# Optimization experiments

Hardware: AMD Instinct MI355X
Metric: run time of the kernel (lower is better)

Reference implementation:

```python
import jax, jax.numpy as jnp
import numpy as np

N = 84          # nodes; N*(N-1)/2 == 3486, hardcoded by LayerNorm shapes
P = 3486        # number of pairwise rows
H = 2048        # h_size
EPS = 1e-5


def _gru_cell(x, h, Wih, Whh, bih, bhh):
    # PyTorch GRUCell math. Wih: [3H, in], Whh: [3H, H]
    gi = x @ Wih.T + bih
    gh = h @ Whh.T + bhh
    ir, iz, inew = jnp.split(gi, 3, axis=1)
    hr, hz, hnew = jnp.split(gh, 3, axis=1)
    r = jax.nn.sigmoid(ir + hr)
    z = jax.nn.sigmoid(iz + hz)
    n = jnp.tanh(inew + r * hnew)
    return (1.0 - z) * n + z * h


def _full_ln(x, w, b):
    # nn.LayerNorm([3486, h]) normalizes over BOTH dims jointly (biased var)
    mu = jnp.mean(x)
    var = jnp.mean((x - mu) ** 2)
    return (x - mu) * jax.lax.rsqrt(var + EPS) * w + b


def setup_inputs() -> dict:
    key = jax.random.key(0)
    ks = jax.random.split(key, 22)
    f32 = jnp.float32

    def nrm(k, shape, std):
        return jax.random.normal(k, shape, dtype=f32) * std

    h2 = H // 2
    return {
        "x": nrm(ks[0], (N, 64), 1.0),
        "hid": nrm(ks[1], (P, H), 1.0),
        # GRUCell(64, H) parameters
        "gru_Wih": nrm(ks[2], (3 * H, 64), 1.0 / np.sqrt(64)),
        "gru_Whh": nrm(ks[3], (3 * H, H), 1.0 / np.sqrt(H)),
        "gru_bih": nrm(ks[4], (3 * H,), 0.01),
        "gru_bhh": nrm(ks[5], (3 * H,), 0.01),
        # Linear/LayerNorm stack
        "W1": nrm(ks[6], (H, H), np.sqrt(2.0 / H)),
        "b1": jnp.zeros((H,), f32),
        "ln1_w": jnp.ones((P, H), f32),
        "ln1_b": jnp.zeros((P, H), f32),
        "W2": nrm(ks[7], (h2, H), np.sqrt(2.0 / H)),
        "b2": jnp.zeros((h2,), f32),
        "ln2_w": jnp.ones((P, h2), f32),
        "ln2_b": jnp.zeros((P, h2), f32),
        "W3": nrm(ks[8], (h2, h2), np.sqrt(2.0 / h2)),
        "b3": jnp.zeros((h2,), f32),
        "ln3_w": jnp.ones((P, h2), f32),
        "ln3_b": jnp.zeros((P, h2), f32),
        "W4": nrm(ks[9], (1, h2), np.sqrt(2.0 / h2)),
        "b4": jnp.zeros((1,), f32),
    }


def reference(x, hid, gru_Wih, gru_Whh, gru_bih, gru_bhh,
              W1, b1, ln1_w, ln1_b, W2, b2, ln2_w, ln2_b,
              W3, b3, ln3_w, ln3_b, W4, b4):
    # Pairwise gather: rows ordered (0,1),(0,2),...,(0,N-1),(1,2),... -- matches
    # the torch loop of expand+cat.
    iu, ju = jnp.triu_indices(N, k=1)
    x1 = x[iu]  # [P, 64]
    x2 = x[ju]  # [P, 64]

    h = _gru_cell(x1, hid, gru_Wih, gru_Whh, gru_bih, gru_bhh)
    h = _gru_cell(x2, h, gru_Wih, gru_Whh, gru_bih, gru_bhh)

    h = _full_ln(jax.nn.relu(h @ W1.T + b1), ln1_w, ln1_b)
    h = _full_ln(jax.nn.relu(h @ W2.T + b2), ln2_w, ln2_b)
    h = _full_ln(jax.nn.relu(h @ W3.T + b3), ln3_w, ln3_b)
    vals = jax.nn.sigmoid(h @ W4.T + b4)[:, 0]  # [P]

    # Strict-upper-triangular scatter + symmetrize (equals the torch pad loop)
    M = jnp.zeros((N, N), dtype=vals.dtype).at[iu, ju].set(vals)
    return M + M.T
```

## Files before the change

kernel.cpp:

```cpp
#include <hip/hip_runtime.h>
#include <stdint.h>

#define P_PAIRS 3486
#define NNODES 84
#define HSZ 2048
#define H2SZ 1024
#define G3H 6144
#define LN_EPS 1e-5f

typedef short bf16x8 __attribute__((ext_vector_type(8)));
typedef float f32x4 __attribute__((ext_vector_type(4)));

typedef __attribute__((address_space(3))) unsigned int lds_uint;
typedef __attribute__((address_space(1))) const unsigned int global_cuint;

__device__ __forceinline__ unsigned short f2bf(float f) {
    unsigned int u = __float_as_uint(f);
    return (unsigned short)((u + 0x7fffu + ((u >> 16) & 1u)) >> 16);
}
__device__ __forceinline__ float bf2f(unsigned short s) {
    return __uint_as_float(((unsigned int)s) << 16);
}
__device__ __forceinline__ float sigm(float x) {
    return 1.f / (1.f + expf(-x));
}

#define S_WHH (G3H * HSZ / 4)
#define S_W1  (HSZ * HSZ / 4)
#define S_W2  (H2SZ * HSZ / 4)
#define S_W3  (H2SZ * H2SZ / 4)
#define S_HID (P_PAIRS * HSZ / 4)
#define B0 (S_WHH)
#define B1 (B0 + S_W1)
#define B2 (B1 + S_W2)
#define B3 (B2 + S_W3)
#define B4 (B3 + S_HID)

__device__ __forceinline__ void cvt4(const float4* in, ushort4* out, int i) {
    float4 v = in[i];
    ushort4 o;
    o.x = f2bf(v.x); o.y = f2bf(v.y); o.z = f2bf(v.z); o.w = f2bf(v.w);
    out[i] = o;
}

__global__ void k_prep(const float4* __restrict__ Whh, ushort4* __restrict__ whh_b,
                       const float4* __restrict__ W1, ushort4* __restrict__ w1_b,
                       const float4* __restrict__ W2, ushort4* __restrict__ w2_b,
                       const float4* __restrict__ W3, ushort4* __restrict__ w3_b,
                       const float4* __restrict__ hid, ushort4* __restrict__ hid_b,
                       int* __restrict__ ip, int* __restrict__ jp, float* __restrict__ acc) {
    int idx = blockIdx.x * blockDim.x + threadIdx.x;
    if (idx < 8) acc[idx] = 0.f;
    if (idx < P_PAIRS) {
        int i = 0, rem = idx;
        while (rem >= NNODES - 1 - i) { rem -= NNODES - 1 - i; ++i; }
        ip[idx] = i;
        jp[idx] = i + 1 + rem;
    }
    int stride = gridDim.x * blockDim.x;
    for (; idx < B4; idx += stride) {
        if (idx < B0)      cvt4(Whh, whh_b, idx);
        else if (idx < B1) cvt4(W1, w1_b, idx - B0);
        else if (idx < B2) cvt4(W2, w2_b, idx - B1);
        else if (idx < B3) cvt4(W3, w3_b, idx - B2);
        else               cvt4(hid, hid_b, idx - B3);
    }
}

__global__ void k_gi(const float* __restrict__ x, const float* __restrict__ Wih,
                     const float* __restrict__ bih, float* __restrict__ gi) {
    int idx = blockIdx.x * blockDim.x + threadIdx.x;
    if (idx >= NNODES * G3H) return;
    int node = idx / G3H, n = idx - node * G3H;
    const float* xr = x + node * 64;
    const float* wr = Wih + (size_t)n * 64;
    float s = bih[n];
#pragma unroll
    for (int k = 0; k < 64; ++k) s += xr[k] * wr[k];
    gi[idx] = s;
}

__global__ __launch_bounds__(256)
void k_gemm(const unsigned short* __restrict__ A, const unsigned short* __restrict__ B,
            const float* __restrict__ bias, float* __restrict__ Cf,
            unsigned short* __restrict__ Cb,
            int M, int N, int K, int relu, float* __restrict__ accg, int redslot) {
    __shared__ __align__(16) unsigned short lsA[128 * 32];
    __shared__ __align__(16) unsigned short lsB[128 * 32];
    const int mt_count = (M + 127) >> 7;
    const int per_group = mt_count << 3;
    const int g = blockIdx.x / per_group;
    const int rr = blockIdx.x - g * per_group;
    const int nt = (g << 3) + (rr & 7);
    const int mt = rr >> 3;
    const int m0 = mt * 128;
    const int n0 = nt * 128;
    const int tid = threadIdx.x;
    const int lane = tid & 63;
    const int wave = tid >> 6;
    const int wr = (wave >> 1) * 64;
    const int wc = (wave & 1) * 64;
    const int fr = lane & 15;
    const int quad = lane >> 4;
    const int kof = quad * 8;

    f32x4 acc[4][4];
#pragma unroll
    for (int i = 0; i < 4; ++i)
#pragma unroll
        for (int j = 0; j < 4; ++j) {
            f32x4 z = {0.f, 0.f, 0.f, 0.f};
            acc[i][j] = z;
        }

    const int lin0 = (wave * 2) * 1024 + lane * 16;
    const int lin1 = lin0 + 1024;
    const int row0 = lin0 >> 6, col0 = (lin0 & 63) >> 1;
    const int row1 = lin1 >> 6, col1 = (lin1 & 63) >> 1;
    int ga0 = m0 + row0; if (ga0 >= M) ga0 = M - 1;
    int ga1 = m0 + row1; if (ga1 >= M) ga1 = M - 1;
    const int gb0 = n0 + row0, gb1 = n0 + row1;

    const unsigned short* pa0 = A + (size_t)ga0 * K + col0;
    const unsigned short* pa1 = A + (size_t)ga1 * K + col1;
    const unsigned short* pb0 = B + (size_t)gb0 * K + col0;
    const unsigned short* pb1 = B + (size_t)gb1 * K + col1;
    lds_uint* la0 = (lds_uint*)&lsA[(wave * 2) * 512];
    lds_uint* la1 = (lds_uint*)&lsA[(wave * 2 + 1) * 512];
    lds_uint* lb0 = (lds_uint*)&lsB[(wave * 2) * 512];
    lds_uint* lb1 = (lds_uint*)&lsB[(wave * 2 + 1) * 512];

    for (int k0 = 0; k0 < K; k0 += 32) {
        __syncthreads();
        __builtin_amdgcn_global_load_lds((global_cuint*)(pa0 + k0), la0, 16, 0, 0);
        __builtin_amdgcn_global_load_lds((global_cuint*)(pa1 + k0), la1, 16, 0, 0);
        __builtin_amdgcn_global_load_lds((global_cuint*)(pb0 + k0), lb0, 16, 0, 0);
        __builtin_amdgcn_global_load_lds((global_cuint*)(pb1 + k0), lb1, 16, 0, 0);
        __syncthreads();
        bf16x8 av[4], bv[4];
#pragma unroll
        for (int mi = 0; mi < 4; ++mi)
            av[mi] = *(const bf16x8*)(&lsA[(wr + mi * 16 + fr) * 32 + kof]);
#pragma unroll
        for (int ni = 0; ni < 4; ++ni)
            bv[ni] = *(const bf16x8*)(&lsB[(wc + ni * 16 + fr) * 32 + kof]);
#pragma unroll
        for (int mi = 0; mi < 4; ++mi)
#pragma unroll
            for (int ni = 0; ni < 4; ++ni)
                acc[mi][ni] = __builtin_amdgcn_mfma_f32_16x16x32_bf16(av[mi], bv[ni], acc[mi][ni], 0, 0, 0);
    }

    float s1 = 0.f, s2 = 0.f;
#pragma unroll
    for (int mi = 0; mi < 4; ++mi) {
#pragma unroll
        for (int r = 0; r < 4; ++r) {
            int row = m0 + wr + mi * 16 + quad * 4 + r;
            if (row >= M) continue;
#pragma unroll
            for (int ni = 0; ni < 4; ++ni) {
                int col = n0 + wc + ni * 16 + fr;
                float v = acc[mi][ni][r];
                if (bias) v += bias[col];
                if (relu) v = fmaxf(v, 0.f);
                if (redslot >= 0) { s1 += v; s2 += v * v; }
                if (Cb) Cb[(size_t)row * N + col] = f2bf(v);
                else    Cf[(size_t)row * N + col] = v;
            }
        }
    }

    if (redslot >= 0) {
        __syncthreads();
        float* sm = (float*)lsA;
        sm[tid] = s1;
        sm[256 + tid] = s2;
        __syncthreads();
        for (int o = 128; o > 0; o >>= 1) {
            if (tid < o) {
                sm[tid] += sm[tid + o];
                sm[256 + tid] += sm[256 + tid + o];
            }
            __syncthreads();
        }
        if (tid == 0) {
            atomicAdd(&accg[redslot * 2], sm[0]);
            atomicAdd(&accg[redslot * 2 + 1], sm[256]);
        }
    }
}

__global__ void k_combine(const float4* __restrict__ gi, const ushort4* __restrict__ gh,
                          const int* __restrict__ pair, const float4* __restrict__ hprev_f,
                          const ushort4* __restrict__ hprev_b,
                          ushort4* __restrict__ hout) {
    int idx = blockIdx.x * blockDim.x + threadIdx.x;
    if (idx >= P_PAIRS * (HSZ / 4)) return;
    int p = idx >> 9;
    int c4 = idx & 511;
    int node = pair[p];
    const float4* gip = gi + (size_t)node * (G3H / 4) + c4;
    const ushort4* ghp = gh + (size_t)p * (G3H / 4) + c4;
    float4 gir = gip[0],   giz = gip[512], gin = gip[1024];
    ushort4 ghr4 = ghp[0], ghz4 = ghp[512], ghn4 = ghp[1024];
    float hr[4] = {bf2f(ghr4.x), bf2f(ghr4.y), bf2f(ghr4.z), bf2f(ghr4.w)};
    float hz[4] = {bf2f(ghz4.x), bf2f(ghz4.y), bf2f(ghz4.z), bf2f(ghz4.w)};
    float hn[4] = {bf2f(ghn4.x), bf2f(ghn4.y), bf2f(ghn4.z), bf2f(ghn4.w)};
    float hp[4];
    if (hprev_f) {
        float4 h = hprev_f[idx];
        hp[0] = h.x; hp[1] = h.y; hp[2] = h.z; hp[3] = h.w;
    } else {
        ushort4 h = hprev_b[idx];
        hp[0] = bf2f(h.x); hp[1] = bf2f(h.y); hp[2] = bf2f(h.z); hp[3] = bf2f(h.w);
    }
    float ir[4] = {gir.x, gir.y, gir.z, gir.w};
    float iz[4] = {giz.x, giz.y, giz.z, giz.w};
    float in_[4] = {gin.x, gin.y, gin.z, gin.w};
    unsigned short o[4];
#pragma unroll
    for (int q = 0; q < 4; ++q) {
        float r = sigm(ir[q] + hr[q]);
        float z = sigm(iz[q] + hz[q]);
        float nn = tanhf(in_[q] + r * hn[q]);
        o[q] = f2bf((1.f - z) * nn + z * hp[q]);
    }
    ushort4 ov = {o[0], o[1], o[2], o[3]};
    hout[idx] = ov;
}

__global__ void k_lnapply(const float4* __restrict__ t, const float4* __restrict__ w,
                          const float4* __restrict__ b, const float* __restrict__ acc, int slot,
                          int n, ushort4* __restrict__ out) {
    float cnt = (float)n;
    float mu = acc[slot * 2] / cnt;
    float var = acc[slot * 2 + 1] / cnt - mu * mu;
    float inv = rsqrtf(var + LN_EPS);
    int n4 = n >> 2;
    int idx = blockIdx.x * blockDim.x + threadIdx.x;
    int stride = gridDim.x * blockDim.x;
    for (; idx < n4; idx += stride) {
        float4 tv = t[idx], wv = w[idx], bv = b[idx];
        ushort4 o;
        o.x = f2bf((tv.x - mu) * inv * wv.x + bv.x);
        o.y = f2bf((tv.y - mu) * inv * wv.y + bv.y);
        o.z = f2bf((tv.z - mu) * inv * wv.z + bv.z);
        o.w = f2bf((tv.w - mu) * inv * wv.w + bv.w);
        out[idx] = o;
    }
}

__global__ void k_head(const float* __restrict__ t, const float* __restrict__ w,
                       const float* __restrict__ b, const float* __restrict__ accv,
                       const float* __restrict__ W4, const float* __restrict__ b4,
                       float* __restrict__ vals) {
    float cnt = (float)P_PAIRS * (float)H2SZ;
    float mu = accv[4] / cnt;
    float var = accv[5] / cnt - mu * mu;
    float inv = rsqrtf(var + LN_EPS);
    int wid = (blockIdx.x * blockDim.x + threadIdx.x) >> 6;
    int lane = threadIdx.x & 63;
    if (wid >= P_PAIRS) return;
    const float* row = t + (size_t)wid * H2SZ;
    const float* wrp = w + (size_t)wid * H2SZ;
    const float* brp = b + (size_t)wid * H2SZ;
    float s = 0.f;
    for (int k = lane; k < H2SZ; k += 64)
        s += ((row[k] - mu) * inv * wrp[k] + brp[k]) * W4[k];
#pragma unroll
    for (int o = 32; o > 0; o >>= 1) s += __shfl_down(s, o, 64);
    if (lane == 0) vals[wid] = sigm(s + b4[0]);
}

__global__ void k_out(const float* __restrict__ vals, float* __restrict__ out) {
    int idx = blockIdx.x * blockDim.x + threadIdx.x;
    if (idx >= NNODES * NNODES) return;
    int r = idx / NNODES, c = idx - r * NNODES;
    if (r == c) { out[idx] = 0.f; return; }
    int i = r < c ? r : c, j = r < c ? c : r;
    int p = i * (NNODES - 1) - i * (i - 1) / 2 + (j - i - 1);
    out[idx] = vals[p];
}

extern "C" void kernel_launch(void* const* d_in, const int* in_sizes, int n_in,
                              void* d_out, int out_size, void* d_ws, size_t ws_size,
                              hipStream_t stream) {
    const float* x    = (const float*)d_in[0];
    const float* hid  = (const float*)d_in[1];
    const float* Wih  = (const float*)d_in[2];
    const float* Whh  = (const float*)d_in[3];
    const float* bih  = (const float*)d_in[4];
    const float* bhh  = (const float*)d_in[5];
    const float* W1   = (const float*)d_in[6];
    const float* b1   = (const float*)d_in[7];
    const float* ln1w = (const float*)d_in[8];
    const float* ln1b = (const float*)d_in[9];
    const float* W2   = (const float*)d_in[10];
    const float* b2   = (const float*)d_in[11];
    const float* ln2w = (const float*)d_in[12];
    const float* ln2b = (const float*)d_in[13];
    const float* W3   = (const float*)d_in[14];
    const float* b3   = (const float*)d_in[15];
    const float* ln3w = (const float*)d_in[16];
    const float* ln3b = (const float*)d_in[17];
    const float* W4   = (const float*)d_in[18];
    const float* b4   = (const float*)d_in[19];
    float* out = (float*)d_out;

    char* ws = (char*)d_ws;
    size_t off = 0;
    auto alloc = [&](size_t bytes) -> void* {
        off = (off + 255) & ~(size_t)255;
        void* p = ws + off;
        off += bytes;
        return p;
    };

    float* acc            = (float*)alloc(8 * sizeof(float));
    int*   ip             = (int*)alloc(P_PAIRS * sizeof(int));
    int*   jp             = (int*)alloc(P_PAIRS * sizeof(int));
    float* gi             = (float*)alloc((size_t)NNODES * G3H * sizeof(float));
    unsigned short* whh_b = (unsigned short*)alloc((size_t)G3H * HSZ * 2);
    unsigned short* w1_b  = (unsigned short*)alloc((size_t)HSZ * HSZ * 2);
    unsigned short* w2_b  = (unsigned short*)alloc((size_t)H2SZ * HSZ * 2);
    unsigned short* w3_b  = (unsigned short*)alloc((size_t)H2SZ * H2SZ * 2);
    unsigned short* hid_b = (unsigned short*)alloc((size_t)P_PAIRS * HSZ * 2);
    unsigned short* hbuf  = (unsigned short*)alloc((size_t)P_PAIRS * HSZ * 2);
    unsigned short* gh    = (unsigned short*)alloc((size_t)P_PAIRS * G3H * 2);
    float* t              = (float*)alloc((size_t)P_PAIRS * HSZ * sizeof(float));
    float* vals           = (float*)alloc((size_t)P_PAIRS * sizeof(float));
    (void)ws_size; (void)in_sizes; (void)n_in; (void)out_size;

    unsigned short* lnb = hid_b;

    k_prep<<<2048, 256, 0, stream>>>((const float4*)Whh, (ushort4*)whh_b,
                                     (const float4*)W1, (ushort4*)w1_b,
                                     (const float4*)W2, (ushort4*)w2_b,
                                     (const float4*)W3, (ushort4*)w3_b,
                                     (const float4*)hid, (ushort4*)hid_b,
                                     ip, jp, acc);
    k_gi<<<(NNODES * G3H + 255) / 256, 256, 0, stream>>>(x, Wih, bih, gi);

    const int MT = (P_PAIRS + 127) / 128;
    int gBig = MT * (G3H / 128);
    int g3   = MT * (HSZ / 128);
    int g4   = MT * (H2SZ / 128);
    int cgrid = (P_PAIRS * HSZ / 4 + 255) / 256;

    k_gemm<<<gBig, 256, 0, stream>>>(hid_b, whh_b, bhh, nullptr, gh, P_PAIRS, G3H, HSZ, 0, acc, -1);
    k_combine<<<cgrid, 256, 0, stream>>>((const float4*)gi, (const ushort4*)gh, ip,
                                         (const float4*)hid, nullptr, (ushort4*)hbuf);
    k_gemm<<<gBig, 256, 0, stream>>>(hbuf, whh_b, bhh, nullptr, gh, P_PAIRS, G3H, HSZ, 0, acc, -1);
    k_combine<<<cgrid, 256, 0, stream>>>((const float4*)gi, (const ushort4*)gh, jp,
                                         nullptr, (const ushort4*)hbuf, (ushort4*)hbuf);

    k_gemm<<<g3, 256, 0, stream>>>(hbuf, w1_b, b1, t, nullptr, P_PAIRS, HSZ, HSZ, 1, acc, 0);
    k_lnapply<<<2048, 256, 0, stream>>>((const float4*)t, (const float4*)ln1w, (const float4*)ln1b,
                                        acc, 0, P_PAIRS * HSZ, (ushort4*)lnb);

    k_gemm<<<g4, 256, 0, stream>>>(lnb, w2_b, b2, t, nullptr, P_PAIRS, H2SZ, HSZ, 1, acc, 1);
    k_lnapply<<<2048, 256, 0, stream>>>((const float4*)t, (const float4*)ln2w, (const float4*)ln2b,
                                        acc, 1, P_PAIRS * H2SZ, (ushort4*)lnb);

    k_gemm<<<g4, 256, 0, stream>>>(lnb, w3_b, b3, t, nullptr, P_PAIRS, H2SZ, H2SZ, 1, acc, 2);

    k_head<<<(P_PAIRS * 64 + 255) / 256, 256, 0, stream>>>(t, ln3w, ln3b, acc, W4, b4, vals);

    k_out<<<(NNODES * NNODES + 255) / 256, 256, 0, stream>>>(vals, out);
}
```

Before: 839.7 us.

## Double-buffer wave-private LDS tiles in GEMM and drop block barriers

The GEMM kernel now gives each wave its own 64-row A and B tiles in LDS and double-buffers them. The next K-slice is prefetched with global_load_lds while MFMAs run on the current slice. Explicit s_waitcnt replaces the per-iteration __syncthreads pairs. The grouped block rasterization is also replaced by a plain 2D grid. In exchange, tiles are no longer shared across waves, which doubles global/L2 load traffic per block, raises LDS use to 64KB per block (lowering occupancy), and gives up the L2-friendly block ordering.

```diff
diff --git a/kernel.cpp b/kernel.cpp
--- a/kernel.cpp
+++ b/kernel.cpp
@@ -13,6 +13,9 @@
 
 typedef __attribute__((address_space(3))) unsigned int lds_uint;
 typedef __attribute__((address_space(1))) const unsigned int global_cuint;
+
+#define WAIT_VM(n) __builtin_amdgcn_s_waitcnt(0x0F00 | 0x70 | ((n) & 0xF) | (((n) >> 4) << 14))
+#define WAIT_LGKM0 __builtin_amdgcn_s_waitcnt(0xC000 | 0x70 | 0xF)
 
 __device__ __forceinline__ unsigned short f2bf(float f) {
     unsigned int u = __float_as_uint(f);
@@ -85,16 +88,9 @@
             const float* __restrict__ bias, float* __restrict__ Cf,
             unsigned short* __restrict__ Cb,
             int M, int N, int K, int relu, float* __restrict__ accg, int redslot) {
-    __shared__ __align__(16) unsigned short lsA[128 * 32];
-    __shared__ __align__(16) unsigned short lsB[128 * 32];
-    const int mt_count = (M + 127) >> 7;
-    const int per_group = mt_count << 3;
-    const int g = blockIdx.x / per_group;
-    const int rr = blockIdx.x - g * per_group;
-    const int nt = (g << 3) + (rr & 7);
-    const int mt = rr >> 3;
-    const int m0 = mt * 128;
-    const int n0 = nt * 128;
+    __shared__ __align__(16) unsigned short lds[4 * 2 * 4096];
+    const int m0 = blockIdx.x * 128;
+    const int n0 = blockIdx.y * 128;
     const int tid = threadIdx.x;
     const int lane = tid & 63;
     const int wave = tid >> 6;
@@ -113,42 +109,55 @@
             acc[i][j] = z;
         }
 
-    const int lin0 = (wave * 2) * 1024 + lane * 16;
-    const int lin1 = lin0 + 1024;
-    const int row0 = lin0 >> 6, col0 = (lin0 & 63) >> 1;
-    const int row1 = lin1 >> 6, col1 = (lin1 & 63) >> 1;
-    int ga0 = m0 + row0; if (ga0 >= M) ga0 = M - 1;
-    int ga1 = m0 + row1; if (ga1 >= M) ga1 = M - 1;
-    const int gb0 = n0 + row0, gb1 = n0 + row1;
-
-    const unsigned short* pa0 = A + (size_t)ga0 * K + col0;
-    const unsigned short* pa1 = A + (size_t)ga1 * K + col1;
-    const unsigned short* pb0 = B + (size_t)gb0 * K + col0;
-    const unsigned short* pb1 = B + (size_t)gb1 * K + col1;
-    lds_uint* la0 = (lds_uint*)&lsA[(wave * 2) * 512];
-    lds_uint* la1 = (lds_uint*)&lsA[(wave * 2 + 1) * 512];
-    lds_uint* lb0 = (lds_uint*)&lsB[(wave * 2) * 512];
-    lds_uint* lb1 = (lds_uint*)&lsB[(wave * 2 + 1) * 512];
-
+    const int lrow = lane >> 2;
+    const int lcol = (lane & 3) * 8;
+    const unsigned short* pa[4];
+    const unsigned short* pb[4];
+#pragma unroll
+    for (int c = 0; c < 4; ++c) {
+        int ga = m0 + wr + c * 16 + lrow; if (ga >= M) ga = M - 1;
+        int gb = n0 + wc + c * 16 + lrow;
+        pa[c] = A + (size_t)ga * K + lcol;
+        pb[c] = B + (size_t)gb * K + lcol;
+    }
+    unsigned short* wbase = &lds[wave * 8192];
+
+#pragma unroll
+    for (int c = 0; c < 4; ++c) {
+        __builtin_amdgcn_global_load_lds((global_cuint*)(pa[c]), (lds_uint*)(wbase + c * 512), 16, 0, 0);
+        __builtin_amdgcn_global_load_lds((global_cuint*)(pb[c]), (lds_uint*)(wbase + 2048 + c * 512), 16, 0, 0);
+    }
+
+    int cur = 0;
     for (int k0 = 0; k0 < K; k0 += 32) {
-        __syncthreads();
-        __builtin_amdgcn_global_load_lds((global_cuint*)(pa0 + k0), la0, 16, 0, 0);
-        __builtin_amdgcn_global_load_lds((global_cuint*)(pa1 + k0), la1, 16, 0, 0);
-        __builtin_amdgcn_global_load_lds((global_cuint*)(pb0 + k0), lb0, 16, 0, 0);
-        __builtin_amdgcn_global_load_lds((global_cuint*)(pb1 + k0), lb1, 16, 0, 0);
-        __syncthreads();
+        const int nxt = cur ^ 1;
+        if (k0 + 32 < K) {
+            WAIT_LGKM0;
+#pragma unroll
+            for (int c = 0; c < 4; ++c) {
+                __builtin_amdgcn_global_load_lds((global_cuint*)(pa[c] + k0 + 32),
+                                                 (lds_uint*)(wbase + nxt * 4096 + c * 512), 16, 0, 0);
+                __builtin_amdgcn_global_load_lds((global_cuint*)(pb[c] + k0 + 32),
+                                                 (lds_uint*)(wbase + nxt * 4096 + 2048 + c * 512), 16, 0, 0);
+            }
+            WAIT_VM(8);
+        } else {
+            WAIT_VM(0);
+        }
+        const unsigned short* buf = wbase + cur * 4096;
         bf16x8 av[4], bv[4];
 #pragma unroll
         for (int mi = 0; mi < 4; ++mi)
-            av[mi] = *(const bf16x8*)(&lsA[(wr + mi * 16 + fr) * 32 + kof]);
+            av[mi] = *(const bf16x8*)(&buf[(mi * 16 + fr) * 32 + kof]);
 #pragma unroll
         for (int ni = 0; ni < 4; ++ni)
-            bv[ni] = *(const bf16x8*)(&lsB[(wc + ni * 16 + fr) * 32 + kof]);
+            bv[ni] = *(const bf16x8*)(&buf[2048 + (ni * 16 + fr) * 32 + kof]);
 #pragma unroll
         for (int mi = 0; mi < 4; ++mi)
 #pragma unroll
             for (int ni = 0; ni < 4; ++ni)
                 acc[mi][ni] = __builtin_amdgcn_mfma_f32_16x16x32_bf16(av[mi], bv[ni], acc[mi][ni], 0, 0, 0);
+        cur = nxt;
     }
 
     float s1 = 0.f, s2 = 0.f;
@@ -173,7 +182,7 @@
 
     if (redslot >= 0) {
         __syncthreads();
-        float* sm = (float*)lsA;
+        float* sm = (float*)lds;
         sm[tid] = s1;
         sm[256 + tid] = s2;
         __syncthreads();
@@ -342,10 +351,9 @@
                                      ip, jp, acc);
     k_gi<<<(NNODES * G3H + 255) / 256, 256, 0, stream>>>(x, Wih, bih, gi);
 
-    const int MT = (P_PAIRS + 127) / 128;
-    int gBig = MT * (G3H / 128);
-    int g3   = MT * (HSZ / 128);
-    int g4   = MT * (H2SZ / 128);
+    dim3 gBig((P_PAIRS + 127) / 128, G3H / 128);
+    dim3 g3((P_PAIRS + 127) / 128, HSZ / 128);
+    dim3 g4((P_PAIRS + 127) / 128, H2SZ / 128);
     int cgrid = (P_PAIRS * HSZ / 4 + 255) / 256;
 
     k_gemm<<<gBig, 256, 0, stream>>>(hid_b, whh_b, bhh, nullptr, gh, P_PAIRS, G3H, HSZ, 0, acc, -1);
```

Result: faster. 822.6 us (-2.0%).

## Fold input-gate GEMV into prep kernel and use plain 2D GEMM grid

Applied to the files above, without the earlier changes.

Merges the k_gi kernel into k_prep as a grid-stride loop, removing one launch. Also drops the grouped (8-wide N super-tile) block swizzle in k_gemm and indexes M/N tiles directly through a 2D grid. Blocks that share a B tile now run at the same time instead of blocks sharing an A tile, which changes L2 reuse. This may raise L2 misses on A, and the fused prep kernel now carries the gi work on a fixed 2048-block grid.

```diff
diff --git a/kernel.cpp b/kernel.cpp
--- a/kernel.cpp
+++ b/kernel.cpp
@@ -48,8 +48,12 @@
                        const float4* __restrict__ W2, ushort4* __restrict__ w2_b,
                        const float4* __restrict__ W3, ushort4* __restrict__ w3_b,
                        const float4* __restrict__ hid, ushort4* __restrict__ hid_b,
-                       int* __restrict__ ip, int* __restrict__ jp, float* __restrict__ acc) {
-    int idx = blockIdx.x * blockDim.x + threadIdx.x;
+                       int* __restrict__ ip, int* __restrict__ jp, float* __restrict__ acc,
+                       const float* __restrict__ x, const float* __restrict__ Wih,
+                       const float* __restrict__ bih, float* __restrict__ gi) {
+    const int tid0 = blockIdx.x * blockDim.x + threadIdx.x;
+    const int stride = gridDim.x * blockDim.x;
+    int idx = tid0;
     if (idx < 8) acc[idx] = 0.f;
     if (idx < P_PAIRS) {
         int i = 0, rem = idx;
@@ -57,7 +61,6 @@
         ip[idx] = i;
         jp[idx] = i + 1 + rem;
     }
-    int stride = gridDim.x * blockDim.x;
     for (; idx < B4; idx += stride) {
         if (idx < B0)      cvt4(Whh, whh_b, idx);
         else if (idx < B1) cvt4(W1, w1_b, idx - B0);
@@ -65,19 +68,15 @@
         else if (idx < B3) cvt4(W3, w3_b, idx - B2);
         else               cvt4(hid, hid_b, idx - B3);
     }
-}
-
-__global__ void k_gi(const float* __restrict__ x, const float* __restrict__ Wih,
-                     const float* __restrict__ bih, float* __restrict__ gi) {
-    int idx = blockIdx.x * blockDim.x + threadIdx.x;
-    if (idx >= NNODES * G3H) return;
-    int node = idx / G3H, n = idx - node * G3H;
-    const float* xr = x + node * 64;
-    const float* wr = Wih + (size_t)n * 64;
-    float s = bih[n];
-#pragma unroll
-    for (int k = 0; k < 64; ++k) s += xr[k] * wr[k];
-    gi[idx] = s;
+    for (int g = tid0; g < NNODES * G3H; g += stride) {
+        int node = g / G3H, n = g - node * G3H;
+        const float* xr = x + node * 64;
+        const float* wr = Wih + (size_t)n * 64;
+        float s = bih[n];
+#pragma unroll
+        for (int k = 0; k < 64; ++k) s += xr[k] * wr[k];
+        gi[g] = s;
+    }
 }
 
 __global__ __launch_bounds__(256)
@@ -87,14 +86,8 @@
             int M, int N, int K, int relu, float* __restrict__ accg, int redslot) {
     __shared__ __align__(16) unsigned short lsA[128 * 32];
     __shared__ __align__(16) unsigned short lsB[128 * 32];
-    const int mt_count = (M + 127) >> 7;
-    const int per_group = mt_count << 3;
-    const int g = blockIdx.x / per_group;
-    const int rr = blockIdx.x - g * per_group;
-    const int nt = (g << 3) + (rr & 7);
-    const int mt = rr >> 3;
-    const int m0 = mt * 128;
-    const int n0 = nt * 128;
+    const int m0 = blockIdx.x * 128;
+    const int n0 = blockIdx.y * 128;
     const int tid = threadIdx.x;
     const int lane = tid & 63;
     const int wave = tid >> 6;
@@ -339,13 +332,11 @@
                                      (const float4*)W2, (ushort4*)w2_b,
                                      (const float4*)W3, (ushort4*)w3_b,
                                      (const float4*)hid, (ushort4*)hid_b,
-                                     ip, jp, acc);
-    k_gi<<<(NNODES * G3H + 255) / 256, 256, 0, stream>>>(x, Wih, bih, gi);
-
-    const int MT = (P_PAIRS + 127) / 128;
-    int gBig = MT * (G3H / 128);
-    int g3   = MT * (HSZ / 128);
-    int g4   = MT * (H2SZ / 128);
+                                     ip, jp, acc, x, Wih, bih, gi);
+
+    dim3 gBig((P_PAIRS + 127) / 128, G3H / 128);
+    dim3 g3((P_PAIRS + 127) / 128, HSZ / 128);
+    dim3 g4((P_PAIRS + 127) / 128, H2SZ / 128);
     int cgrid = (P_PAIRS * HSZ / 4 + 255) / 256;
 
     k_gemm<<<gBig, 256, 0, stream>>>(hid_b, whh_b, bhh, nullptr, gh, P_PAIRS, G3H, HSZ, 0, acc, -1);
```

Result: no change. 828.4 us (-1.4%).
